# Performance work log

Measured on AMD Instinct MI355X. Metric: run time of the kernel, lower is better.

The kernel has to match this reference:

```python
import jax, jax.numpy as jnp
import numpy as np

DIM = 1024
HID = 4096
E = 8
K = 3


def setup_inputs() -> dict:
    key = jax.random.key(0)
    ks = jax.random.split(key, 5)
    x = jax.random.normal(ks[0], (2, 2048, DIM), dtype=jnp.float32)
    # router: nn.Linear(dim, E) -- initialized to zero in source, but we use small
    # random weights so routing is non-degenerate for the correctness baseline.
    router_w = jax.random.normal(ks[1], (E, DIM), dtype=jnp.float32) * 0.02
    router_b = jax.random.normal(ks[2], (E,), dtype=jnp.float32) * 0.02
    # per-expert SwiGLU params: w12: [E, dim, 2*hid], w3: [E, hid, dim]
    w12 = jax.random.normal(ks[3], (E, DIM, 2 * HID), dtype=jnp.float32) * 0.02
    w3 = jax.random.normal(ks[4], (E, HID, DIM), dtype=jnp.float32) * 0.02
    return {"x": x, "router_w": router_w, "router_b": router_b, "w12": w12, "w3": w3}


def _moe(x, router_w, router_b, w12, w3):
    # router logits [B, S, E]
    logits = jnp.einsum("bsd,ed->bse", x, router_w) + router_b
    scores = jax.nn.sigmoid(logits)
    topk_scores, topk_idx = jax.lax.top_k(scores, K)  # [B,S,K]
    weights = topk_scores / (topk_scores.sum(axis=-1, keepdims=True) + 1e-6)
    # dense per-expert combine weight [B, S, E] (zero if expert not selected)
    onehot = jax.nn.one_hot(topk_idx, E, dtype=x.dtype)  # [B,S,K,E]
    dense_w = jnp.einsum("bske,bsk->bse", onehot, weights)
    out = jnp.zeros_like(x)
    for e in range(E):  # small fixed structural loop over experts
        x12 = x @ w12[e]  # [B,S,2H]
        x1, x2 = jnp.split(x12, 2, axis=-1)
        hidden = jax.nn.silu(x1) * x2
        out = out + (hidden @ w3[e]) * dense_w[..., e:e + 1]
    aux_loss = 0.01 * jnp.mean(logits ** 2)
    return out, aux_loss


def reference(x, router_w, router_b, w12, w3):
    return _moe(x, router_w, router_b, w12, w3)
```

## Files before the change

### kernel.cpp

```cpp
#include <hip/hip_runtime.h>
#include <math.h>

typedef unsigned short u16;
typedef __bf16 bf16x8 __attribute__((ext_vector_type(8)));
typedef float f32x4 __attribute__((ext_vector_type(4)));

#define T_TOK 4096
#define DIM   1024
#define HID   4096
#define NE    8
#define TOPK  3
#define NPAIR 12288

constexpr size_t OFF_CTRL = 0;
constexpr size_t OFF_XB   = 256;
constexpr size_t OFF_W12T = OFF_XB   + (size_t)T_TOK * DIM * 2;
constexpr size_t OFF_W3T  = OFF_W12T + (size_t)NE * 2 * HID * DIM * 2;
constexpr size_t OFF_HID  = OFF_W3T  + (size_t)NE * DIM * HID * 2;
constexpr size_t OFF_Y    = OFF_HID  + (size_t)NPAIR * HID * 2;
constexpr size_t OFF_PTOK = OFF_Y    + (size_t)NPAIR * DIM * 4;
constexpr size_t OFF_TE   = OFF_PTOK + (size_t)NPAIR * 4;
constexpr size_t OFF_TW   = OFF_TE   + (size_t)T_TOK * TOPK * 4;
constexpr size_t OFF_TS   = OFF_TW   + (size_t)T_TOK * TOPK * 4;

__device__ __forceinline__ u16 f2bf(float f) {
    unsigned u = __builtin_bit_cast(unsigned, f);
    u += 0x7fffu + ((u >> 16) & 1u);
    return (u16)(u >> 16);
}

__device__ __forceinline__ void ld_g2l(const u16* g, u16* l) {
    __builtin_amdgcn_global_load_lds((__attribute__((address_space(1))) unsigned*)(g),
                                     (__attribute__((address_space(3))) unsigned*)(l),
                                     16, 0, 0);
}

#define VMCNT(N) asm volatile("s_waitcnt vmcnt(" #N ")" ::: "memory")
#define LGKM0  asm volatile("s_waitcnt lgkmcnt(0)" ::: "memory")
#define SBAR   __builtin_amdgcn_s_barrier()
#define SCHED0 __builtin_amdgcn_sched_barrier(0)
#define PRIO1  __builtin_amdgcn_s_setprio(1)
#define PRIO0  __builtin_amdgcn_s_setprio(0)

#define STAGE_A02(dst) { ld_g2l(srcA[0], (dst) + (0 * 64 + wave * 8) * 64); \
                         ld_g2l(srcA[2], (dst) + (2 * 64 + wave * 8) * 64); }
#define STAGE_B01(dst) { ld_g2l(srcB[0], (dst) + 16384 + (0 * 64 + wave * 8) * 64); \
                         ld_g2l(srcB[1], (dst) + 16384 + (1 * 64 + wave * 8) * 64); }
#define STAGE_B23(dst) { ld_g2l(srcB[2], (dst) + 16384 + (2 * 64 + wave * 8) * 64); \
                         ld_g2l(srcB[3], (dst) + 16384 + (3 * 64 + wave * 8) * 64); }
#define STAGE_A13(dst) { ld_g2l(srcA[1], (dst) + (1 * 64 + wave * 8) * 64); \
                         ld_g2l(srcA[3], (dst) + (3 * 64 + wave * 8) * 64); }
#define ADV()          { _Pragma("unroll") \
                         for (int r_ = 0; r_ < 4; ++r_) { srcA[r_] += 64; srcB[r_] += 64; } }

__global__ __launch_bounds__(256) void transpose_cast_kernel(const float* __restrict__ in,
                                                             u16* __restrict__ out, int K, int N) {
    __shared__ float tile[64][33];
    const float* inp = in + (size_t)blockIdx.z * K * N;
    u16* outp = out + (size_t)blockIdx.z * K * N;
    const int n0 = blockIdx.x * 32, k0 = blockIdx.y * 64;
    const int tid = threadIdx.x;
#pragma unroll
    for (int i = 0; i < 2; ++i) {
        int k = i * 32 + (tid >> 3);
        int c4 = (tid & 7) * 4;
        float4 f = *(const float4*)(inp + (size_t)(k0 + k) * N + n0 + c4);
        tile[k][c4 + 0] = f.x; tile[k][c4 + 1] = f.y;
        tile[k][c4 + 2] = f.z; tile[k][c4 + 3] = f.w;
    }
    __syncthreads();
    const int n = tid >> 3, c = (tid & 7) * 8;
    u16 buf[8];
#pragma unroll
    for (int j = 0; j < 8; ++j) buf[j] = f2bf(tile[c + j][n]);
    *(uint4*)(outp + (size_t)(n0 + n) * K + k0 + c) = *(uint4*)buf;
}

__global__ __launch_bounds__(256) void router_kernel(const float* __restrict__ x,
                                                     const float* __restrict__ rw,
                                                     const float* __restrict__ rb,
                                                     u16* __restrict__ xb,
                                                     int* __restrict__ tok_expert,
                                                     float* __restrict__ tok_w,
                                                     int* __restrict__ ctrl,
                                                     float* __restrict__ aux) {
    __shared__ int hist[NE];
    __shared__ float auxsh;
    const int tid = threadIdx.x;
    if (tid < NE) hist[tid] = 0;
    if (tid == NE) auxsh = 0.f;
    __syncthreads();

    const int wave = tid >> 6, lane = tid & 63;
    const int t = blockIdx.x * 4 + wave;
    const float* xr = x + (size_t)t * DIM;
    u16* xbr = xb + (size_t)t * DIM;

    float p[NE];
#pragma unroll
    for (int e = 0; e < NE; e++) p[e] = 0.f;
#pragma unroll
    for (int q = 0; q < 4; ++q) {
        const int d = q * 256 + lane * 4;
        float4 f = *(const float4*)(xr + d);
        uint2 v;
        v.x = (unsigned)f2bf(f.x) | ((unsigned)f2bf(f.y) << 16);
        v.y = (unsigned)f2bf(f.z) | ((unsigned)f2bf(f.w) << 16);
        *(uint2*)(xbr + d) = v;
#pragma unroll
        for (int e = 0; e < NE; e++) {
            float4 w = *(const float4*)(rw + e * DIM + d);
            p[e] += f.x * w.x + f.y * w.y + f.z * w.z + f.w * w.w;
        }
    }
#pragma unroll
    for (int e = 0; e < NE; e++) {
#pragma unroll
        for (int off = 32; off; off >>= 1) p[e] += __shfl_down(p[e], off, 64);
    }
    if (lane == 0) {
        float s[NE]; float auxs = 0.f;
#pragma unroll
        for (int e = 0; e < NE; e++) {
            float lg = p[e] + rb[e];
            auxs += lg * lg;
            s[e] = 1.f / (1.f + __expf(-lg));
        }
        atomicAdd(&auxsh, auxs);
        unsigned mask = 0; float wsum = 0.f;
        int idxs[TOPK]; float vals[TOPK];
        for (int k = 0; k < TOPK; k++) {
            float best = -1.f; int bi = 0;
            for (int e = 0; e < NE; e++)
                if (!((mask >> e) & 1u) && s[e] > best) { best = s[e]; bi = e; }
            mask |= 1u << bi; idxs[k] = bi; vals[k] = best; wsum += best;
        }
        wsum += 1e-6f;
        for (int k = 0; k < TOPK; k++) {
            tok_expert[t * TOPK + k] = idxs[k];
            tok_w[t * TOPK + k] = vals[k] / wsum;
            atomicAdd(&hist[idxs[k]], 1);
        }
    }
    __syncthreads();
    if (tid < NE) { int h = hist[tid]; if (h) atomicAdd(&ctrl[tid], h); }
    if (tid == NE) atomicAdd(aux, auxsh * (0.01f / 32768.0f));
}

__global__ void scan_kernel(int* __restrict__ ctrl) {
    if (threadIdx.x == 0) {
        int acc = 0;
        for (int e = 0; e < NE; e++) { ctrl[8 + e] = acc; acc += ctrl[e]; }
    }
}

__global__ __launch_bounds__(256) void assign_kernel(const int* __restrict__ tok_expert,
                                                     const float* __restrict__ tok_w,
                                                     int* __restrict__ ctrl,
                                                     int* __restrict__ pair_token,
                                                     int* __restrict__ tok_slot) {
    int t = blockIdx.x * blockDim.x + threadIdx.x;
    if (t >= T_TOK) return;
    for (int k = 0; k < TOPK; k++) {
        int e = tok_expert[t * TOPK + k];
        int pos = atomicAdd(&ctrl[16 + e], 1);
        int slot = ctrl[8 + e] + pos;
        pair_token[slot] = t;
        tok_slot[t * TOPK + k] = slot;
    }
}

__global__ __launch_bounds__(512, 2) void gemm1_kernel(const u16* __restrict__ xb,
                                                       const u16* __restrict__ w12t,
                                                       const int* __restrict__ pair_token,
                                                       const int* __restrict__ ctrl,
                                                       u16* __restrict__ hidden) {
    const int e = blockIdx.z;
    const int cnt = ctrl[e];
    if ((int)blockIdx.y * 256 >= cnt) return;
    const int off = ctrl[8 + e];
    const int rowbase = off + blockIdx.y * 256;
    const int rowend = off + cnt;
    const int n0 = blockIdx.x * 128;

    extern __shared__ __align__(16) u16 lds[];

    const int tid = threadIdx.x;
    const int wave = tid >> 6, lane = tid & 63;
    const int srow = tid >> 3;
    const int scol = ((tid & 7) ^ (srow & 7)) * 8;

    const u16* srcA[4];
    const u16* srcB[4];
#pragma unroll
    for (int r = 0; r < 4; ++r) {
        int sr = rowbase + r * 64 + srow;
        int tok = (sr < rowend) ? pair_token[sr] : 0;
        srcA[r] = xb + (size_t)tok * DIM + scol;
    }
#pragma unroll
    for (int r = 0; r < 2; ++r) {
        srcB[r]     = w12t + ((size_t)e * 2 * HID + n0 + r * 64 + srow) * DIM + scol;
        srcB[r + 2] = srcB[r] + (size_t)HID * DIM;
    }

    const int wm = wave >> 2, wn = wave & 3;
    const int lrow = lane & 15, lq = lane >> 4, xm = lrow & 7;
    const int so0 = ((lq ^ xm) << 3);
    const int so1 = (((4 | lq) ^ xm) << 3);

    f32x4 acc0[8][2], acc1[8][2];
#pragma unroll
    for (int mf = 0; mf < 8; ++mf)
#pragma unroll
        for (int nf = 0; nf < 2; ++nf) { acc0[mf][nf] = (f32x4)0.f; acc1[mf][nf] = (f32x4)0.f; }

    STAGE_A02(lds); STAGE_B01(lds);
    STAGE_B23(lds);
    STAGE_A13(lds);
    ADV();

    const int NT = DIM / 64;
    for (int kt = 0; kt < NT; ++kt) {
        u16* cur = lds + (kt & 1) * 32768;
        u16* nxt = lds + ((kt & 1) ^ 1) * 32768;
        const u16* sA = cur;
        const u16* sB = cur + 16384;
        const bool notlast = (kt < NT - 1);

        bf16x8 a[4][2], b0[2][2], b1[2][2];
        VMCNT(4); SBAR; SCHED0;
#pragma unroll
        for (int mf = 0; mf < 4; ++mf) {
            const u16* base = sA + (wm * 128 + mf * 16 + lrow) * 64;
            a[mf][0] = *(const bf16x8*)(base + so0);
            a[mf][1] = *(const bf16x8*)(base + so1);
        }
#pragma unroll
        for (int nf = 0; nf < 2; ++nf) {
            const u16* base = sB + (wn * 32 + nf * 16 + lrow) * 64;
            b0[nf][0] = *(const bf16x8*)(base + so0);
            b0[nf][1] = *(const bf16x8*)(base + so1);
        }
        if (notlast) { STAGE_A02(nxt); STAGE_B01(nxt); }
        LGKM0; SCHED0;
        PRIO1;
#pragma unroll
        for (int mf = 0; mf < 4; ++mf)
#pragma unroll
            for (int nf = 0; nf < 2; ++nf) {
                acc0[mf][nf] = __builtin_amdgcn_mfma_f32_16x16x32_bf16(a[mf][0], b0[nf][0], acc0[mf][nf], 0, 0, 0);
                acc0[mf][nf] = __builtin_amdgcn_mfma_f32_16x16x32_bf16(a[mf][1], b0[nf][1], acc0[mf][nf], 0, 0, 0);
            }
        PRIO0;
        if (notlast) { VMCNT(6); } else { VMCNT(2); }
        SBAR; SCHED0;
#pragma unroll
        for (int nf = 0; nf < 2; ++nf) {
            const u16* base = sB + 128 * 64 + (wn * 32 + nf * 16 + lrow) * 64;
            b1[nf][0] = *(const bf16x8*)(base + so0);
            b1[nf][1] = *(const bf16x8*)(base + so1);
        }
        if (notlast) STAGE_B23(nxt);
        LGKM0; SCHED0;
        PRIO1;
#pragma unroll
        for (int mf = 0; mf < 4; ++mf)
#pragma unroll
            for (int nf = 0; nf < 2; ++nf) {
                acc1[mf][nf] = __builtin_amdgcn_mfma_f32_16x16x32_bf16(a[mf][0], b1[nf][0], acc1[mf][nf], 0, 0, 0);
                acc1[mf][nf] = __builtin_amdgcn_mfma_f32_16x16x32_bf16(a[mf][1], b1[nf][1], acc1[mf][nf], 0, 0, 0);
            }
        PRIO0;
        if (notlast) { VMCNT(6); } else { VMCNT(0); }
        SBAR; SCHED0;
#pragma unroll
        for (int mf = 0; mf < 4; ++mf) {
            const u16* base = sA + (wm * 128 + (mf + 4) * 16 + lrow) * 64;
            a[mf][0] = *(const bf16x8*)(base + so0);
            a[mf][1] = *(const bf16x8*)(base + so1);
        }
        if (notlast) { STAGE_A13(nxt); ADV(); }
        LGKM0; SCHED0;
        PRIO1;
#pragma unroll
        for (int mf = 0; mf < 4; ++mf)
#pragma unroll
            for (int nf = 0; nf < 2; ++nf) {
                acc1[mf + 4][nf] = __builtin_amdgcn_mfma_f32_16x16x32_bf16(a[mf][0], b1[nf][0], acc1[mf + 4][nf], 0, 0, 0);
                acc1[mf + 4][nf] = __builtin_amdgcn_mfma_f32_16x16x32_bf16(a[mf][1], b1[nf][1], acc1[mf + 4][nf], 0, 0, 0);
            }
        PRIO0;
        SBAR;
        PRIO1;
#pragma unroll
        for (int mf = 0; mf < 4; ++mf)
#pragma unroll
            for (int nf = 0; nf < 2; ++nf) {
                acc0[mf + 4][nf] = __builtin_amdgcn_mfma_f32_16x16x32_bf16(a[mf][0], b0[nf][0], acc0[mf + 4][nf], 0, 0, 0);
                acc0[mf + 4][nf] = __builtin_amdgcn_mfma_f32_16x16x32_bf16(a[mf][1], b0[nf][1], acc0[mf + 4][nf], 0, 0, 0);
            }
        PRIO0;
    }

#pragma unroll
    for (int mf = 0; mf < 8; ++mf) {
        const int gr0 = rowbase + wm * 128 + mf * 16 + lq * 4;
#pragma unroll
        for (int nf = 0; nf < 2; ++nf) {
            const int gc = n0 + wn * 32 + nf * 16 + lrow;
#pragma unroll
            for (int r = 0; r < 4; ++r) {
                const int gr = gr0 + r;
                if (gr < rowend) {
                    float x1 = acc0[mf][nf][r], x2 = acc1[mf][nf][r];
                    float h = x1 / (1.f + __expf(-x1)) * x2;
                    hidden[(size_t)gr * HID + gc] = f2bf(h);
                }
            }
        }
    }
}

__global__ __launch_bounds__(512, 2) void gemm2_kernel(const u16* __restrict__ hidden,
                                                       const u16* __restrict__ w3t,
                                                       const int* __restrict__ ctrl,
                                                       float* __restrict__ ybuf) {
    const int e = blockIdx.z;
    const int cnt = ctrl[e];
    if ((int)blockIdx.y * 256 >= cnt) return;
    const int off = ctrl[8 + e];
    const int rowbase = off + blockIdx.y * 256;
    const int rowend = off + cnt;
    const int n0 = blockIdx.x * 256;

    extern __shared__ __align__(16) u16 lds[];

    const int tid = threadIdx.x;
    const int wave = tid >> 6, lane = tid & 63;
    const int srow = tid >> 3;
    const int scol = ((tid & 7) ^ (srow & 7)) * 8;

    const u16* srcA[4];
    const u16* srcB[4];
#pragma unroll
    for (int r = 0; r < 4; ++r) {
        int sr = rowbase + r * 64 + srow;
        if (sr > NPAIR - 1) sr = NPAIR - 1;
        srcA[r] = hidden + (size_t)sr * HID + scol;
        srcB[r] = w3t + ((size_t)e * DIM + n0 + r * 64 + srow) * HID + scol;
    }

    const int wm = wave >> 2, wn = wave & 3;
    const int lrow = lane & 15, lq = lane >> 4, xm = lrow & 7;
    const int so0 = ((lq ^ xm) << 3);
    const int so1 = (((4 | lq) ^ xm) << 3);

    f32x4 acc[8][4];
#pragma unroll
    for (int mf = 0; mf < 8; ++mf)
#pragma unroll
        for (int nf = 0; nf < 4; ++nf) acc[mf][nf] = (f32x4)0.f;

    STAGE_A02(lds); STAGE_B01(lds);
    STAGE_B23(lds);
    STAGE_A13(lds);
    ADV();

    const int NT = HID / 64;
    for (int kt = 0; kt < NT; ++kt) {
        u16* cur = lds + (kt & 1) * 32768;
        u16* nxt = lds + ((kt & 1) ^ 1) * 32768;
        const u16* sA = cur;
        const u16* sB = cur + 16384;
        const bool notlast = (kt < NT - 1);

        bf16x8 a[4][2], b[4][2];
        VMCNT(4); SBAR; SCHED0;
#pragma unroll
        for (int mf = 0; mf < 4; ++mf) {
            const u16* base = sA + (wm * 128 + mf * 16 + lrow) * 64;
            a[mf][0] = *(const bf16x8*)(base + so0);
            a[mf][1] = *(const bf16x8*)(base + so1);
        }
#pragma unroll
        for (int nf = 0; nf < 2; ++nf) {
            const u16* base = sB + (nf * 64 + wn * 16 + lrow) * 64;
            b[nf][0] = *(const bf16x8*)(base + so0);
            b[nf][1] = *(const bf16x8*)(base + so1);
        }
        if (notlast) { STAGE_A02(nxt); STAGE_B01(nxt); }
        LGKM0; SCHED0;
        PRIO1;
#pragma unroll
        for (int mf = 0; mf < 4; ++mf)
#pragma unroll
            for (int nf = 0; nf < 2; ++nf) {
                acc[mf][nf] = __builtin_amdgcn_mfma_f32_16x16x32_bf16(a[mf][0], b[nf][0], acc[mf][nf], 0, 0, 0);
                acc[mf][nf] = __builtin_amdgcn_mfma_f32_16x16x32_bf16(a[mf][1], b[nf][1], acc[mf][nf], 0, 0, 0);
            }
        PRIO0;
        if (notlast) { VMCNT(6); } else { VMCNT(2); }
        SBAR; SCHED0;
#pragma unroll
        for (int nf = 2; nf < 4; ++nf) {
            const u16* base = sB + (nf * 64 + wn * 16 + lrow) * 64;
            b[nf][0] = *(const bf16x8*)(base + so0);
            b[nf][1] = *(const bf16x8*)(base + so1);
        }
        if (notlast) STAGE_B23(nxt);
        LGKM0; SCHED0;
        PRIO1;
#pragma unroll
        for (int mf = 0; mf < 4; ++mf)
#pragma unroll
            for (int nf = 2; nf < 4; ++nf) {
                acc[mf][nf] = __builtin_amdgcn_mfma_f32_16x16x32_bf16(a[mf][0], b[nf][0], acc[mf][nf], 0, 0, 0);
                acc[mf][nf] = __builtin_amdgcn_mfma_f32_16x16x32_bf16(a[mf][1], b[nf][1], acc[mf][nf], 0, 0, 0);
            }
        PRIO0;
        if (notlast) { VMCNT(6); } else { VMCNT(0); }
        SBAR; SCHED0;
#pragma unroll
        for (int mf = 0; mf < 4; ++mf) {
            const u16* base = sA + (wm * 128 + (mf + 4) * 16 + lrow) * 64;
            a[mf][0] = *(const bf16x8*)(base + so0);
            a[mf][1] = *(const bf16x8*)(base + so1);
        }
        if (notlast) { STAGE_A13(nxt); ADV(); }
        LGKM0; SCHED0;
        PRIO1;
#pragma unroll
        for (int mf = 0; mf < 4; ++mf)
#pragma unroll
            for (int nf = 2; nf < 4; ++nf) {
                acc[mf + 4][nf] = __builtin_amdgcn_mfma_f32_16x16x32_bf16(a[mf][0], b[nf][0], acc[mf + 4][nf], 0, 0, 0);
                acc[mf + 4][nf] = __builtin_amdgcn_mfma_f32_16x16x32_bf16(a[mf][1], b[nf][1], acc[mf + 4][nf], 0, 0, 0);
            }
        PRIO0;
        SBAR;
        PRIO1;
#pragma unroll
        for (int mf = 0; mf < 4; ++mf)
#pragma unroll
            for (int nf = 0; nf < 2; ++nf) {
                acc[mf + 4][nf] = __builtin_amdgcn_mfma_f32_16x16x32_bf16(a[mf][0], b[nf][0], acc[mf + 4][nf], 0, 0, 0);
                acc[mf + 4][nf] = __builtin_amdgcn_mfma_f32_16x16x32_bf16(a[mf][1], b[nf][1], acc[mf + 4][nf], 0, 0, 0);
            }
        PRIO0;
    }

#pragma unroll
    for (int mf = 0; mf < 8; ++mf) {
        const int gr0 = rowbase + wm * 128 + mf * 16 + lq * 4;
#pragma unroll
        for (int nf = 0; nf < 4; ++nf) {
            const int gc = n0 + nf * 64 + wn * 16 + lrow;
#pragma unroll
            for (int r = 0; r < 4; ++r) {
                const int gr = gr0 + r;
                if (gr < rowend) ybuf[(size_t)gr * DIM + gc] = acc[mf][nf][r];
            }
        }
    }
}

__global__ __launch_bounds__(256) void combine_kernel(const float* __restrict__ ybuf,
                                                      const int* __restrict__ tok_slot,
                                                      const float* __restrict__ tok_w,
                                                      float* __restrict__ out) {
    const int t = blockIdx.x;
    const int d = threadIdx.x * 4;
    const int s0 = tok_slot[t * 3 + 0], s1 = tok_slot[t * 3 + 1], s2 = tok_slot[t * 3 + 2];
    const float w0 = tok_w[t * 3 + 0], w1 = tok_w[t * 3 + 1], w2 = tok_w[t * 3 + 2];
    const float4 a0 = *(const float4*)(ybuf + (size_t)s0 * DIM + d);
    const float4 a1 = *(const float4*)(ybuf + (size_t)s1 * DIM + d);
    const float4 a2 = *(const float4*)(ybuf + (size_t)s2 * DIM + d);
    float4 o;
    o.x = w0 * a0.x + w1 * a1.x + w2 * a2.x;
    o.y = w0 * a0.y + w1 * a1.y + w2 * a2.y;
    o.z = w0 * a0.z + w1 * a1.z + w2 * a2.z;
    o.w = w0 * a0.w + w1 * a1.w + w2 * a2.w;
    *(float4*)(out + (size_t)t * DIM + d) = o;
}

extern "C" void kernel_launch(void* const* d_in, const int* in_sizes, int n_in,
                              void* d_out, int out_size, void* d_ws, size_t ws_size,
                              hipStream_t stream) {
    const float* x   = (const float*)d_in[0];
    const float* rw  = (const float*)d_in[1];
    const float* rb  = (const float*)d_in[2];
    const float* w12 = (const float*)d_in[3];
    const float* w3  = (const float*)d_in[4];
    float* out = (float*)d_out;
    char* ws = (char*)d_ws;

    int*   ctrl       = (int*)(ws + OFF_CTRL);
    u16*   xb         = (u16*)(ws + OFF_XB);
    u16*   w12t       = (u16*)(ws + OFF_W12T);
    u16*   w3t        = (u16*)(ws + OFF_W3T);
    u16*   hidden     = (u16*)(ws + OFF_HID);
    float* ybuf       = (float*)(ws + OFF_Y);
    int*   pair_token = (int*)(ws + OFF_PTOK);
    int*   tok_expert = (int*)(ws + OFF_TE);
    float* tok_w      = (float*)(ws + OFF_TW);
    int*   tok_slot   = (int*)(ws + OFF_TS);

    static bool attr_set = false;
    if (!attr_set) {
        hipFuncSetAttribute((const void*)gemm1_kernel, hipFuncAttributeMaxDynamicSharedMemorySize, 131072);
        hipFuncSetAttribute((const void*)gemm2_kernel, hipFuncAttributeMaxDynamicSharedMemorySize, 131072);
        attr_set = true;
    }

    hipMemsetAsync(ctrl, 0, 256, stream);
    hipMemsetAsync(out + (size_t)T_TOK * DIM, 0, sizeof(float), stream);

    router_kernel<<<T_TOK / 4, 256, 0, stream>>>(x, rw, rb, xb, tok_expert, tok_w, ctrl,
                                                 out + (size_t)T_TOK * DIM);
    transpose_cast_kernel<<<dim3(2 * HID / 32, DIM / 64, NE), 256, 0, stream>>>(w12, w12t, DIM, 2 * HID);
    transpose_cast_kernel<<<dim3(DIM / 32, HID / 64, NE), 256, 0, stream>>>(w3, w3t, HID, DIM);
    scan_kernel<<<1, 64, 0, stream>>>(ctrl);
    assign_kernel<<<16, 256, 0, stream>>>(tok_expert, tok_w, ctrl, pair_token, tok_slot);

    gemm1_kernel<<<dim3(HID / 128, 16, NE), 512, 131072, stream>>>(xb, w12t, pair_token, ctrl, hidden);
    gemm2_kernel<<<dim3(DIM / 256, 16, NE), 512, 131072, stream>>>(hidden, w3t, ctrl, ybuf);
    combine_kernel<<<T_TOK, 256, 0, stream>>>(ybuf, tok_slot, tok_w, out);
    (void)in_sizes; (void)n_in; (void)out_size; (void)ws_size;
}
```

Baseline: 894.5 us.

## Drop scan kernel and remove explicit sched barriers and lgkm waits in GEMMs

Removes the single-thread scan kernel launch and has assign and the GEMM kernels compute expert prefix offsets inline from the counts. Also deletes the explicit lgkmcnt(0) waits and sched_barrier fences in both GEMM main loops, leaving the compiler to schedule LDS reads and MFMAs and insert waits itself. This saves one tiny launch, but the compiler may reorder or serialise MFMAs differently from the hand-tuned schedule, which could hurt the carefully interleaved pipeline.

```diff
diff --git a/kernel.cpp b/kernel.cpp
--- a/kernel.cpp
+++ b/kernel.cpp
@@ -36,9 +36,7 @@
 }
 
 #define VMCNT(N) asm volatile("s_waitcnt vmcnt(" #N ")" ::: "memory")
-#define LGKM0  asm volatile("s_waitcnt lgkmcnt(0)" ::: "memory")
 #define SBAR   __builtin_amdgcn_s_barrier()
-#define SCHED0 __builtin_amdgcn_sched_barrier(0)
 #define PRIO1  __builtin_amdgcn_s_setprio(1)
 #define PRIO0  __builtin_amdgcn_s_setprio(0)
 
@@ -147,24 +145,24 @@
     if (tid == NE) atomicAdd(aux, auxsh * (0.01f / 32768.0f));
 }
 
-__global__ void scan_kernel(int* __restrict__ ctrl) {
-    if (threadIdx.x == 0) {
-        int acc = 0;
-        for (int e = 0; e < NE; e++) { ctrl[8 + e] = acc; acc += ctrl[e]; }
-    }
-}
-
 __global__ __launch_bounds__(256) void assign_kernel(const int* __restrict__ tok_expert,
                                                      const float* __restrict__ tok_w,
                                                      int* __restrict__ ctrl,
                                                      int* __restrict__ pair_token,
                                                      int* __restrict__ tok_slot) {
+    __shared__ int soff[NE];
+    if (threadIdx.x < NE) {
+        int acc = 0;
+        for (int i = 0; i < (int)threadIdx.x; ++i) acc += ctrl[i];
+        soff[threadIdx.x] = acc;
+    }
+    __syncthreads();
     int t = blockIdx.x * blockDim.x + threadIdx.x;
     if (t >= T_TOK) return;
     for (int k = 0; k < TOPK; k++) {
         int e = tok_expert[t * TOPK + k];
         int pos = atomicAdd(&ctrl[16 + e], 1);
-        int slot = ctrl[8 + e] + pos;
+        int slot = soff[e] + pos;
         pair_token[slot] = t;
         tok_slot[t * TOPK + k] = slot;
     }
@@ -178,7 +176,8 @@
     const int e = blockIdx.z;
     const int cnt = ctrl[e];
     if ((int)blockIdx.y * 256 >= cnt) return;
-    const int off = ctrl[8 + e];
+    int off = 0;
+    for (int i = 0; i < e; ++i) off += ctrl[i];
     const int rowbase = off + blockIdx.y * 256;
     const int rowend = off + cnt;
     const int n0 = blockIdx.x * 128;
@@ -229,7 +228,7 @@
         const bool notlast = (kt < NT - 1);
 
         bf16x8 a[4][2], b0[2][2], b1[2][2];
-        VMCNT(4); SBAR; SCHED0;
+        VMCNT(4); SBAR;
 #pragma unroll
         for (int mf = 0; mf < 4; ++mf) {
             const u16* base = sA + (wm * 128 + mf * 16 + lrow) * 64;
@@ -243,7 +242,6 @@
             b0[nf][1] = *(const bf16x8*)(base + so1);
         }
         if (notlast) { STAGE_A02(nxt); STAGE_B01(nxt); }
-        LGKM0; SCHED0;
         PRIO1;
 #pragma unroll
         for (int mf = 0; mf < 4; ++mf)
@@ -254,7 +252,7 @@
             }
         PRIO0;
         if (notlast) { VMCNT(6); } else { VMCNT(2); }
-        SBAR; SCHED0;
+        SBAR;
 #pragma unroll
         for (int nf = 0; nf < 2; ++nf) {
             const u16* base = sB + 128 * 64 + (wn * 32 + nf * 16 + lrow) * 64;
@@ -262,7 +260,6 @@
             b1[nf][1] = *(const bf16x8*)(base + so1);
         }
         if (notlast) STAGE_B23(nxt);
-        LGKM0; SCHED0;
         PRIO1;
 #pragma unroll
         for (int mf = 0; mf < 4; ++mf)
@@ -273,7 +270,7 @@
             }
         PRIO0;
         if (notlast) { VMCNT(6); } else { VMCNT(0); }
-        SBAR; SCHED0;
+        SBAR;
 #pragma unroll
         for (int mf = 0; mf < 4; ++mf) {
             const u16* base = sA + (wm * 128 + (mf + 4) * 16 + lrow) * 64;
@@ -281,7 +278,6 @@
             a[mf][1] = *(const bf16x8*)(base + so1);
         }
         if (notlast) { STAGE_A13(nxt); ADV(); }
-        LGKM0; SCHED0;
         PRIO1;
 #pragma unroll
         for (int mf = 0; mf < 4; ++mf)
@@ -329,7 +325,8 @@
     const int e = blockIdx.z;
     const int cnt = ctrl[e];
     if ((int)blockIdx.y * 256 >= cnt) return;
-    const int off = ctrl[8 + e];
+    int off = 0;
+    for (int i = 0; i < e; ++i) off += ctrl[i];
     const int rowbase = off + blockIdx.y * 256;
     const int rowend = off + cnt;
     const int n0 = blockIdx.x * 256;
@@ -376,7 +373,7 @@
         const bool notlast = (kt < NT - 1);
 
         bf16x8 a[4][2], b[4][2];
-        VMCNT(4); SBAR; SCHED0;
+        VMCNT(4); SBAR;
 #pragma unroll
         for (int mf = 0; mf < 4; ++mf) {
             const u16* base = sA + (wm * 128 + mf * 16 + lrow) * 64;
@@ -390,7 +387,6 @@
             b[nf][1] = *(const bf16x8*)(base + so1);
         }
         if (notlast) { STAGE_A02(nxt); STAGE_B01(nxt); }
-        LGKM0; SCHED0;
         PRIO1;
 #pragma unroll
         for (int mf = 0; mf < 4; ++mf)
@@ -401,7 +397,7 @@
             }
         PRIO0;
         if (notlast) { VMCNT(6); } else { VMCNT(2); }
-        SBAR; SCHED0;
+        SBAR;
 #pragma unroll
         for (int nf = 2; nf < 4; ++nf) {
             const u16* base = sB + (nf * 64 + wn * 16 + lrow) * 64;
@@ -409,7 +405,6 @@
             b[nf][1] = *(const bf16x8*)(base + so1);
         }
         if (notlast) STAGE_B23(nxt);
-        LGKM0; SCHED0;
         PRIO1;
 #pragma unroll
         for (int mf = 0; mf < 4; ++mf)
@@ -420,7 +415,7 @@
             }
         PRIO0;
         if (notlast) { VMCNT(6); } else { VMCNT(0); }
-        SBAR; SCHED0;
+        SBAR;
 #pragma unroll
         for (int mf = 0; mf < 4; ++mf) {
             const u16* base = sA + (wm * 128 + (mf + 4) * 16 + lrow) * 64;
@@ -428,7 +423,6 @@
             a[mf][1] = *(const bf16x8*)(base + so1);
         }
         if (notlast) { STAGE_A13(nxt); ADV(); }
-        LGKM0; SCHED0;
         PRIO1;
 #pragma unroll
         for (int mf = 0; mf < 4; ++mf)
@@ -520,7 +514,6 @@
                                                  out + (size_t)T_TOK * DIM);
     transpose_cast_kernel<<<dim3(2 * HID / 32, DIM / 64, NE), 256, 0, stream>>>(w12, w12t, DIM, 2 * HID);
     transpose_cast_kernel<<<dim3(DIM / 32, HID / 64, NE), 256, 0, stream>>>(w3, w3t, HID, DIM);
-    scan_kernel<<<1, 64, 0, stream>>>(ctrl);
     assign_kernel<<<16, 256, 0, stream>>>(tok_expert, tok_w, ctrl, pair_token, tok_slot);
 
     gemm1_kernel<<<dim3(HID / 128, 16, NE), 512, 131072, stream>>>(xb, w12t, pair_token, ctrl, hidden);
```

New measurement: 879.6 us. Within noise of the previous version (-1.7%).
